# Kernel tuning notes

Measured on AMD Instinct MI355X. Metric: run time of the kernel, lower is better.

The kernel has to match this reference:

```python
import jax, jax.numpy as jnp
import numpy as np

EPS = 1e-5

def setup_inputs() -> dict:
    key = jax.random.key(0)
    ks = jax.random.split(key, 8)
    B, C, H, W = 8, 128, 128, 128
    return {
        "x1": jax.random.normal(ks[0], (B, C, H, W), jnp.float32),
        "x2": jax.random.normal(ks[1], (B, C, H, W), jnp.float32),
        "se_w1": jax.random.normal(ks[2], (C // 4, 2 * C), jnp.float32) * 0.05,
        "se_w2": jax.random.normal(ks[3], (2 * C, C // 4), jnp.float32) * 0.05,
        "conv_w": jax.random.normal(ks[4], (C, 2 * C, 3, 3), jnp.float32) * 0.05,
        "bn_gamma": jnp.ones((C,), jnp.float32),
        "bn_beta": jnp.zeros((C,), jnp.float32),
        "bn_mean": jax.random.normal(ks[5], (C,), jnp.float32) * 0.1,
        "bn_var": jax.random.uniform(ks[6], (C,), jnp.float32, 0.5, 1.5),
        "gamma": jax.random.uniform(ks[7], (1,), jnp.float32),
    }

def reference(x1, x2, se_w1, se_w2, conv_w, bn_gamma, bn_beta, bn_mean, bn_var, gamma):
    B, C, H, W = x1.shape
    x = jnp.concatenate([x1, x2], axis=1)                      # [B,2C,H,W]
    # SE gate: global avg pool -> Linear/ReLU/Linear/Sigmoid
    avg = jnp.mean(x, axis=(2, 3))                             # [B,2C]
    h = jax.nn.relu(avg @ se_w1.T)                             # [B,C//4]
    se = jax.nn.sigmoid(h @ se_w2.T)                           # [B,2C]
    x = x * se[:, :, None, None]
    # ConvBNReLU (3x3, pad 1, eval-mode BN)
    x = jax.lax.conv_general_dilated(
        x, conv_w, window_strides=(1, 1), padding="SAME",
        dimension_numbers=("NCHW", "OIHW", "NCHW"))           # [B,C,H,W]
    inv = bn_gamma / jnp.sqrt(bn_var + EPS)
    x = jax.nn.relu(x * inv[None, :, None, None]
                    + (bn_beta - bn_mean * inv)[None, :, None, None])
    # Channel self-attention with max-subtraction trick
    q = x.reshape(B, C, H * W)                                 # query = key = value
    sim = jnp.einsum("bcn,bdn->bcd", q, q)                     # [B,C,C]
    sim = jnp.max(sim, axis=-1, keepdims=True) - sim
    sim = jax.nn.softmax(sim, axis=-1)
    feat = jnp.einsum("bcd,bdn->bcn", sim, q).reshape(B, C, H, W)
    return gamma * feat + x
```

## Files before the change

kernel.cpp:

```cpp
#include <hip/hip_runtime.h>
#include <math.h>

#define B_   8
#define C_   128
#define C2_  256
#define H_   128
#define W_   128
#define HW_  16384
#define CR_  32
#define EPS_ 1e-5f
#define NS_  32

typedef _Float16 f16;
typedef f16 f16x8 __attribute__((ext_vector_type(8)));
typedef f16 f16x4 __attribute__((ext_vector_type(4)));
typedef float f32x4 __attribute__((ext_vector_type(4)));

__global__ __launch_bounds__(256) void prep_kernel(
    const float* __restrict__ x1, const float* __restrict__ x2,
    float* __restrict__ avg_sums, f16* __restrict__ xs)
{
    __shared__ f16 T[W_ * 136];
    __shared__ float part[C2_];
    int h = blockIdx.x, b = blockIdx.y;
    int tid = threadIdx.x;
    part[tid] = 0.f;
    f16* out = xs + ((size_t)b * H_ + h) * W_ * C2_;
    for (int p = 0; p < 2; ++p) {
        const float* src = p ? x2 : x1;
        __syncthreads();
        for (int idx = tid; idx < C_ * 32; idx += 256) {
            int c = idx >> 5, w4 = (idx & 31) << 2;
            const float4 v = *(const float4*)&src[(((size_t)b * C_ + c) * H_ + h) * W_ + w4];
            float s = v.x + v.y + v.z + v.w;
            s += __shfl_xor(s, 1, 64);  s += __shfl_xor(s, 2, 64);
            s += __shfl_xor(s, 4, 64);  s += __shfl_xor(s, 8, 64);
            s += __shfl_xor(s, 16, 64);
            if ((tid & 31) == 0) part[p * C_ + c] = s;
            int cs = c ^ (8 * ((idx & 31) & 15));
            T[(w4 + 0) * 136 + cs] = (f16)v.x;
            T[(w4 + 1) * 136 + cs] = (f16)v.y;
            T[(w4 + 2) * 136 + cs] = (f16)v.z;
            T[(w4 + 3) * 136 + cs] = (f16)v.w;
        }
        __syncthreads();
        for (int u = tid; u < W_ * 16; u += 256) {
            int w = u >> 4, o = u & 15;
            f16x8 v = *(const f16x8*)&T[w * 136 + ((o * 8) ^ (8 * ((w >> 2) & 15)))];
            *(f16x8*)&out[w * C2_ + p * C_ + o * 8] = v;
        }
    }
    __syncthreads();
    atomicAdd(&avg_sums[b * C2_ + tid], part[tid]);
}

__global__ __launch_bounds__(256) void se_mlp_kernel(
    const float* __restrict__ avg_sums, const float* __restrict__ w1,
    const float* __restrict__ w2, float* __restrict__ se)
{
    __shared__ float s_avg[B_ * C2_];
    __shared__ float s_h[B_ * CR_];
    for (int i = threadIdx.x; i < B_ * C2_; i += 256)
        s_avg[i] = avg_sums[i] * (1.f / (float)HW_);
    __syncthreads();
    {
        int i = threadIdx.x;
        int b = i / CR_, j = i % CR_;
        float s = 0.f;
        for (int k = 0; k < C2_; ++k) s += s_avg[b * C2_ + k] * w1[j * C2_ + k];
        s_h[i] = fmaxf(s, 0.f);
    }
    __syncthreads();
    for (int i = threadIdx.x; i < B_ * C2_; i += 256) {
        int b = i / C2_, c = i % C2_;
        float s = 0.f;
        #pragma unroll
        for (int j = 0; j < CR_; ++j) s += s_h[b * CR_ + j] * w2[c * CR_ + j];
        se[i] = 1.f / (1.f + expf(-s));
    }
}

__global__ __launch_bounds__(256) void wt_build_kernel(
    const float* __restrict__ conv_w, f16* __restrict__ wt)
{
    int idx = blockIdx.x * 256 + threadIdx.x;
    int ci = idx & 31;
    int co = (idx >> 5) & 127;
    int cc = (idx >> 12) & 7;
    int t  = idx >> 15;
    wt[idx] = (f16)conv_w[((size_t)co * C2_ + cc * 32 + ci) * 9 + t];
}

__global__ __launch_bounds__(256, 2) void conv_mfma_kernel(
    const f16* __restrict__ xs, const f16* __restrict__ wt,
    const float* __restrict__ se,
    const float* __restrict__ bn_gamma, const float* __restrict__ bn_beta,
    const float* __restrict__ bn_mean, const float* __restrict__ bn_var,
    f16* __restrict__ yh, f16* __restrict__ yt)
{
    __shared__ f16 Xs[17408];
    __shared__ __align__(16) f16 seh[C2_];
    int h0 = blockIdx.x * 2, b = blockIdx.y;
    int tid = threadIdx.x;
    int wave = tid >> 6, lane = tid & 63;
    int wn = wave;
    int lr = lane & 15, kg = lane >> 4;
    const f16* xsb = xs + (size_t)b * ((size_t)H_ * W_ * C2_);

    seh[tid] = (f16)se[b * C2_ + tid];

    f32x4 acc[2][8][2];
    #pragma unroll
    for (int o = 0; o < 2; ++o)
        #pragma unroll
        for (int i = 0; i < 8; ++i)
            #pragma unroll
            for (int j = 0; j < 2; ++j)
                #pragma unroll
                for (int r = 0; r < 4; ++r) acc[o][i][j][r] = 0.f;

    f16x8 afb[2][8];
    auto ldaf = [&](int cc, int t, f16x8* dst) {
        const f16* wb = wt + ((size_t)(t * 8 + cc) * C_) * 32;
        #pragma unroll
        for (int i = 0; i < 8; ++i)
            dst[i] = *(const f16x8*)&wb[(i * 16 + lr) * 32 + kg * 8];
    };

    for (int cc = 0; cc < 8; ++cc) {
        __syncthreads();
        ldaf(cc, 0, afb[0]);
        for (int u = tid; u < 4 * 130 * 4; u += 256) {
            int r = u / 520;
            int rem = u - r * 520;
            int col = rem >> 2, q = rem & 3;
            int gh = h0 - 1 + r, gw = col - 1;
            f16x8 v;
            #pragma unroll
            for (int z = 0; z < 8; ++z) v[z] = (f16)0.f;
            if ((unsigned)gh < (unsigned)H_ && (unsigned)gw < (unsigned)W_) {
                v = *(const f16x8*)&xsb[((size_t)(gh * W_ + gw)) * C2_ + cc * 32 + q * 8];
                f16x8 sv = *(const f16x8*)&seh[cc * 32 + q * 8];
                v = v * sv;
            }
            *(f16x8*)&Xs[((r * 4 + q) * 132 + col) * 8] = v;
        }
        __syncthreads();
        #pragma unroll
        for (int t = 0; t < 9; ++t) {
            const int dh = t / 3, dw = t % 3;
            if (t < 8) ldaf(cc, t + 1, afb[(t + 1) & 1]);
            const f16x8* af = afb[t & 1];
            #pragma unroll
            for (int o = 0; o < 2; ++o) {
                int r = o + dh;
                f16x8 bf[2];
                #pragma unroll
                for (int j = 0; j < 2; ++j)
                    bf[j] = *(const f16x8*)&Xs[((r * 4 + kg) * 132 +
                                (wn * 32 + j * 16 + lr + dw)) * 8];
                #pragma unroll
                for (int i = 0; i < 8; ++i)
                    #pragma unroll
                    for (int j = 0; j < 2; ++j)
                        acc[o][i][j] = __builtin_amdgcn_mfma_f32_16x16x32_f16(
                            af[i], bf[j], acc[o][i][j], 0, 0, 0);
            }
        }
    }
    #pragma unroll
    for (int o = 0; o < 2; ++o) {
        __syncthreads();
        #pragma unroll
        for (int i = 0; i < 8; ++i) {
            int cb = i * 16 + kg * 4;
            float inv[4], add[4];
            #pragma unroll
            for (int r = 0; r < 4; ++r) {
                int c = cb + r;
                inv[r] = bn_gamma[c] * rsqrtf(bn_var[c] + EPS_);
                add[r] = bn_beta[c] - bn_mean[c] * inv[r];
            }
            #pragma unroll
            for (int j = 0; j < 2; ++j) {
                int n = wn * 32 + j * 16 + lr;
                f16x4 tv;
                #pragma unroll
                for (int r = 0; r < 4; ++r) {
                    float v = fmaxf(acc[o][i][j][r] * inv[r] + add[r], 0.f);
                    tv[r] = (f16)v;
                    yh[((size_t)b * C_ + cb + r) * HW_ + (h0 + o) * W_ + n] = (f16)v;
                }
                *(f16x4*)&Xs[n * 136 + cb] = tv;
            }
        }
        __syncthreads();
        for (int u = tid; u < 128 * 16; u += 256) {
            int n = u >> 4, o8 = u & 15;
            f16x8 v = *(const f16x8*)&Xs[n * 136 + o8 * 8];
            *(f16x8*)&yt[((size_t)b * HW_ + (h0 + o) * W_ + n) * C_ + o8 * 8] = v;
        }
    }
}

__global__ __launch_bounds__(512) void sim_mfma_kernel(
    const f16* __restrict__ yh, float* __restrict__ simp)
{
    int ns = blockIdx.x, b = blockIdx.y;
    int tid = threadIdx.x, wave = tid >> 6, lane = tid & 63;
    int wm = wave >> 2, wn = wave & 3;
    int lr = lane & 15, kg = lane >> 4;
    const f16* Y = yh + (size_t)b * C_ * HW_;
    int n0 = ns * (HW_ / NS_);

    f32x4 acc[4][2];
    #pragma unroll
    for (int i = 0; i < 4; ++i)
        #pragma unroll
        for (int j = 0; j < 2; ++j)
            #pragma unroll
            for (int r = 0; r < 4; ++r) acc[i][j][r] = 0.f;

    for (int kk = 0; kk < 16; ++kk) {
        int k = n0 + kk * 32 + kg * 8;
        f16x8 af[4], bf[2];
        #pragma unroll
        for (int i = 0; i < 4; ++i)
            af[i] = *(const f16x8*)&Y[(size_t)(wm * 64 + i * 16 + lr) * HW_ + k];
        #pragma unroll
        for (int j = 0; j < 2; ++j)
            bf[j] = *(const f16x8*)&Y[(size_t)(wn * 32 + j * 16 + lr) * HW_ + k];
        #pragma unroll
        for (int i = 0; i < 4; ++i)
            #pragma unroll
            for (int j = 0; j < 2; ++j)
                acc[i][j] = __builtin_amdgcn_mfma_f32_16x16x32_f16(af[i], bf[j], acc[i][j], 0, 0, 0);
    }
    float* dst = simp + (size_t)(ns * B_ + b) * C_ * C_;
    #pragma unroll
    for (int i = 0; i < 4; ++i)
        #pragma unroll
        for (int j = 0; j < 2; ++j)
            #pragma unroll
            for (int r = 0; r < 4; ++r)
                dst[(wm * 64 + i * 16 + kg * 4 + r) * C_ + wn * 32 + j * 16 + lr] = acc[i][j][r];
}

__global__ __launch_bounds__(128) void softmax_kernel(
    const float* __restrict__ simp, f16* __restrict__ Ph)
{
    int bc = blockIdx.x;
    int b = bc / C_;
    int d = threadIdx.x;
    float s = 0.f;
    for (int ns = 0; ns < NS_; ++ns)
        s += simp[((size_t)(ns * B_ + b) * C_ + (bc % C_)) * C_ + d];
    float v = -s;
    float m = v;
    #pragma unroll
    for (int off = 32; off > 0; off >>= 1) m = fmaxf(m, __shfl_xor(m, off, 64));
    __shared__ float sm[2], ss[2];
    int wid = threadIdx.x >> 6;
    if ((threadIdx.x & 63) == 0) sm[wid] = m;
    __syncthreads();
    m = fmaxf(sm[0], sm[1]);
    float p = expf(v - m);
    float sum = p;
    #pragma unroll
    for (int off = 32; off > 0; off >>= 1) sum += __shfl_xor(sum, off, 64);
    if ((threadIdx.x & 63) == 0) ss[wid] = sum;
    __syncthreads();
    sum = ss[0] + ss[1];
    Ph[(size_t)bc * C_ + d] = (f16)(p / sum);
}

__global__ __launch_bounds__(256) void feat_mfma_kernel(
    const f16* __restrict__ Ph, const f16* __restrict__ yt,
    const f16* __restrict__ yh,
    const float* __restrict__ gamma, float* __restrict__ out)
{
    int nt = blockIdx.x, b = blockIdx.y;
    int tid = threadIdx.x, wave = tid >> 6, lane = tid & 63;
    int wm = wave >> 1, wn = wave & 1;
    int lr = lane & 15, kg = lane >> 4;
    int n0 = nt * 128;
    const f16* Pb = Ph + (size_t)b * C_ * C_;
    const f16* Yt = yt + (size_t)b * HW_ * C_;

    f32x4 acc[4][4];
    #pragma unroll
    for (int i = 0; i < 4; ++i)
        #pragma unroll
        for (int j = 0; j < 4; ++j)
            #pragma unroll
            for (int r = 0; r < 4; ++r) acc[i][j][r] = 0.f;

    #pragma unroll
    for (int kk = 0; kk < 4; ++kk) {
        int k = kk * 32 + kg * 8;
        f16x8 af[4], bf[4];
        #pragma unroll
        for (int i = 0; i < 4; ++i)
            af[i] = *(const f16x8*)&Pb[(wm * 64 + i * 16 + lr) * C_ + k];
        #pragma unroll
        for (int j = 0; j < 4; ++j)
            bf[j] = *(const f16x8*)&Yt[(size_t)(n0 + wn * 64 + j * 16 + lr) * C_ + k];
        #pragma unroll
        for (int i = 0; i < 4; ++i)
            #pragma unroll
            for (int j = 0; j < 4; ++j)
                acc[i][j] = __builtin_amdgcn_mfma_f32_16x16x32_f16(af[i], bf[j], acc[i][j], 0, 0, 0);
    }
    float g = gamma[0];
    #pragma unroll
    for (int i = 0; i < 4; ++i) {
        int cb = wm * 64 + i * 16 + kg * 4;
        #pragma unroll
        for (int j = 0; j < 4; ++j) {
            int n = n0 + wn * 64 + j * 16 + lr;
            #pragma unroll
            for (int r = 0; r < 4; ++r) {
                float res = (float)yh[((size_t)b * C_ + cb + r) * HW_ + n];
                out[((size_t)b * C_ + cb + r) * HW_ + n] = g * acc[i][j][r] + res;
            }
        }
    }
}

extern "C" void kernel_launch(void* const* d_in, const int* in_sizes, int n_in,
                              void* d_out, int out_size, void* d_ws, size_t ws_size,
                              hipStream_t stream)
{
    const float* x1       = (const float*)d_in[0];
    const float* x2       = (const float*)d_in[1];
    const float* se_w1    = (const float*)d_in[2];
    const float* se_w2    = (const float*)d_in[3];
    const float* conv_w   = (const float*)d_in[4];
    const float* bn_gamma = (const float*)d_in[5];
    const float* bn_beta  = (const float*)d_in[6];
    const float* bn_mean  = (const float*)d_in[7];
    const float* bn_var   = (const float*)d_in[8];
    const float* gamma    = (const float*)d_in[9];
    float* out = (float*)d_out;

    char* ws = (char*)d_ws;
    float* avg  = (float*)(ws);
    float* se   = (float*)(ws + 8192);
    f16*   Ph   = (f16*)  (ws + 16384);
    f16*   wt   = (f16*)  (ws + 278528);
    f16*   xs   = (f16*)  (ws + 1048576);
    float* simp = (float*)(ws + 1048576);
    f16*   yh   = (f16*)  (ws + 68157440);
    f16*   yt   = (f16*)  (ws + 101711872);

    hipMemsetAsync(avg, 0, B_ * C2_ * sizeof(float), stream);
    prep_kernel<<<dim3(H_, B_), 256, 0, stream>>>(x1, x2, avg, xs);
    se_mlp_kernel<<<dim3(1), 256, 0, stream>>>(avg, se_w1, se_w2, se);
    wt_build_kernel<<<dim3(1152), 256, 0, stream>>>(conv_w, wt);
    conv_mfma_kernel<<<dim3(H_ / 2, B_), 256, 0, stream>>>(
        xs, wt, se, bn_gamma, bn_beta, bn_mean, bn_var, yh, yt);
    sim_mfma_kernel<<<dim3(NS_, B_), 512, 0, stream>>>(yh, simp);
    softmax_kernel<<<dim3(B_ * C_), 128, 0, stream>>>(simp, Ph);
    feat_mfma_kernel<<<dim3(HW_ / 128, B_), 256, 0, stream>>>(Ph, yt, yh, gamma, out);
}
```

Measured before the change: 389.0 us.

## Stage conv weights in LDS and compute four output rows per block

Adds a new 512-thread conv kernel that copies all 9 taps of each 32-channel weight chunk into padded shared memory. Each block computes 4 output rows, and each wave owns one row and half the width, so weight reads are reused across rows instead of reloaded from global memory per wave. It reorders the packed weight layout to cc-major to match. The yt output is now written directly as f16x4 stores instead of going through an LDS transpose, and the old kernel stays as a fallback if the large dynamic LDS request is refused. The roughly 142KB LDS request limits occupancy to one block per CU, and the non-coalesced yt stores could cost bandwidth.

```diff
diff --git a/kernel.cpp b/kernel.cpp
--- a/kernel.cpp
+++ b/kernel.cpp
@@ -86,9 +86,115 @@
     int idx = blockIdx.x * 256 + threadIdx.x;
     int ci = idx & 31;
     int co = (idx >> 5) & 127;
-    int cc = (idx >> 12) & 7;
-    int t  = idx >> 15;
+    int tt = idx >> 12;
+    int cc = tt / 9, t = tt - cc * 9;
     wt[idx] = (f16)conv_w[((size_t)co * C2_ + cc * 32 + ci) * 9 + t];
+}
+
+#define WS_F16  46080
+#define XS_F16  24960
+#define SMEM_BYTES 142592
+
+__global__ __launch_bounds__(512, 2) void conv_mfma_big(
+    const f16* __restrict__ xs, const f16* __restrict__ wt,
+    const float* __restrict__ se,
+    const float* __restrict__ bn_gamma, const float* __restrict__ bn_beta,
+    const float* __restrict__ bn_mean, const float* __restrict__ bn_var,
+    f16* __restrict__ yh, f16* __restrict__ yt)
+{
+    extern __shared__ __align__(16) f16 smem[];
+    f16* Ws  = smem;
+    f16* Xs  = smem + WS_F16;
+    f16* seh = smem + WS_F16 + XS_F16;
+
+    int h0 = blockIdx.x * 4, b = blockIdx.y;
+    int tid = threadIdx.x;
+    int wave = tid >> 6, lane = tid & 63;
+    int orow = wave >> 1, nh = wave & 1;
+    int lr = lane & 15, kg = lane >> 4;
+    const f16* xsb = xs + (size_t)b * ((size_t)H_ * W_ * C2_);
+    const f16* wtb = wt;
+
+    if (tid < 256) seh[tid] = (f16)se[b * C2_ + tid];
+
+    f32x4 acc[8][4];
+    #pragma unroll
+    for (int i = 0; i < 8; ++i)
+        #pragma unroll
+        for (int j = 0; j < 4; ++j)
+            #pragma unroll
+            for (int r = 0; r < 4; ++r) acc[i][j][r] = 0.f;
+
+    for (int cc = 0; cc < 8; ++cc) {
+        __syncthreads();
+        {
+            const f16* wsrc = wtb + (size_t)cc * (9 * 128 * 32);
+            for (int u = tid; u < 4608; u += 512) {
+                int kgu = u & 3, co = (u >> 2) & 127, t = u >> 9;
+                f16x8 w = *(const f16x8*)&wsrc[(t * 128 + co) * 32 + kgu * 8];
+                *(f16x8*)&Ws[(t * 128 + co) * 40 + kgu * 8] = w;
+            }
+        }
+        for (int u = tid; u < 3120; u += 512) {
+            int r = u / 520;
+            int rem = u - r * 520;
+            int col = rem >> 2, q = rem & 3;
+            int gh = h0 - 1 + r, gw = col - 1;
+            f16x8 v;
+            #pragma unroll
+            for (int z = 0; z < 8; ++z) v[z] = (f16)0.f;
+            if ((unsigned)gh < (unsigned)H_ && (unsigned)gw < (unsigned)W_) {
+                v = *(const f16x8*)&xsb[((size_t)(gh * W_ + gw)) * C2_ + cc * 32 + q * 8];
+                f16x8 sv = *(const f16x8*)&seh[cc * 32 + q * 8];
+                v = v * sv;
+            }
+            *(f16x8*)&Xs[((r * 4 + q) * 130 + col) * 8] = v;
+        }
+        __syncthreads();
+        #pragma unroll
+        for (int t = 0; t < 9; ++t) {
+            const int dh = t / 3, dw = t % 3;
+            const int rr = orow + dh;
+            f16x8 af[8], bf[4];
+            #pragma unroll
+            for (int i = 0; i < 8; ++i)
+                af[i] = *(const f16x8*)&Ws[(t * 128 + i * 16 + lr) * 40 + kg * 8];
+            #pragma unroll
+            for (int j = 0; j < 4; ++j)
+                bf[j] = *(const f16x8*)&Xs[((rr * 4 + kg) * 130 +
+                            (nh * 64 + j * 16 + lr + dw)) * 8];
+            #pragma unroll
+            for (int i = 0; i < 8; ++i)
+                #pragma unroll
+                for (int j = 0; j < 4; ++j)
+                    acc[i][j] = __builtin_amdgcn_mfma_f32_16x16x32_f16(
+                        af[i], bf[j], acc[i][j], 0, 0, 0);
+        }
+    }
+    int h = h0 + orow;
+    #pragma unroll
+    for (int i = 0; i < 8; ++i) {
+        int cb = i * 16 + kg * 4;
+        float inv[4], add[4];
+        #pragma unroll
+        for (int r = 0; r < 4; ++r) {
+            int c = cb + r;
+            inv[r] = bn_gamma[c] * rsqrtf(bn_var[c] + EPS_);
+            add[r] = bn_beta[c] - bn_mean[c] * inv[r];
+        }
+        #pragma unroll
+        for (int j = 0; j < 4; ++j) {
+            int n = nh * 64 + j * 16 + lr;
+            f16x4 tv;
+            #pragma unroll
+            for (int r = 0; r < 4; ++r) {
+                float v = fmaxf(acc[i][j][r] * inv[r] + add[r], 0.f);
+                tv[r] = (f16)v;
+                yh[((size_t)b * C_ + cb + r) * HW_ + h * W_ + n] = (f16)v;
+            }
+            *(f16x4*)&yt[((size_t)b * HW_ + h * W_ + n) * C_ + cb] = tv;
+        }
+    }
 }
 
 __global__ __launch_bounds__(256, 2) void conv_mfma_kernel(
@@ -121,7 +227,7 @@
 
     f16x8 afb[2][8];
     auto ldaf = [&](int cc, int t, f16x8* dst) {
-        const f16* wb = wt + ((size_t)(t * 8 + cc) * C_) * 32;
+        const f16* wb = wt + ((size_t)(cc * 9 + t) * C_) * 32;
         #pragma unroll
         for (int i = 0; i < 8; ++i)
             dst[i] = *(const f16x8*)&wb[(i * 16 + lr) * 32 + kg * 8];
@@ -170,7 +276,6 @@
     }
     #pragma unroll
     for (int o = 0; o < 2; ++o) {
-        __syncthreads();
         #pragma unroll
         for (int i = 0; i < 8; ++i) {
             int cb = i * 16 + kg * 4;
@@ -191,14 +296,8 @@
                     tv[r] = (f16)v;
                     yh[((size_t)b * C_ + cb + r) * HW_ + (h0 + o) * W_ + n] = (f16)v;
                 }
-                *(f16x4*)&Xs[n * 136 + cb] = tv;
-            }
-        }
-        __syncthreads();
-        for (int u = tid; u < 128 * 16; u += 256) {
-            int n = u >> 4, o8 = u & 15;
-            f16x8 v = *(const f16x8*)&Xs[n * 136 + o8 * 8];
-            *(f16x8*)&yt[((size_t)b * HW_ + (h0 + o) * W_ + n) * C_ + o8 * 8] = v;
+                *(f16x4*)&yt[((size_t)b * HW_ + (h0 + o) * W_ + n) * C_ + cb] = tv;
+            }
         }
     }
 }
@@ -357,8 +456,18 @@
     prep_kernel<<<dim3(H_, B_), 256, 0, stream>>>(x1, x2, avg, xs);
     se_mlp_kernel<<<dim3(1), 256, 0, stream>>>(avg, se_w1, se_w2, se);
     wt_build_kernel<<<dim3(1152), 256, 0, stream>>>(conv_w, wt);
-    conv_mfma_kernel<<<dim3(H_ / 2, B_), 256, 0, stream>>>(
-        xs, wt, se, bn_gamma, bn_beta, bn_mean, bn_var, yh, yt);
+
+    hipError_t aerr = hipFuncSetAttribute(
+        (const void*)conv_mfma_big,
+        hipFuncAttributeMaxDynamicSharedMemorySize, SMEM_BYTES);
+    if (aerr == hipSuccess) {
+        conv_mfma_big<<<dim3(H_ / 4, B_), 512, SMEM_BYTES, stream>>>(
+            xs, wt, se, bn_gamma, bn_beta, bn_mean, bn_var, yh, yt);
+    } else {
+        conv_mfma_kernel<<<dim3(H_ / 2, B_), 256, 0, stream>>>(
+            xs, wt, se, bn_gamma, bn_beta, bn_mean, bn_var, yh, yt);
+    }
+
     sim_mfma_kernel<<<dim3(NS_, B_), 512, 0, stream>>>(yh, simp);
     softmax_kernel<<<dim3(B_ * C_), 128, 0, stream>>>(simp, Ph);
     feat_mfma_kernel<<<dim3(HW_ / 128, B_), 256, 0, stream>>>(Ph, yt, yh, gamma, out);
```

Result: no change. 394.4 us (+1.4%).

## Stage conv weights in LDS with 4-row tiles and register prefetch; fuse weight repack

Applied to the files above, without the earlier changes.

The conv kernel now handles four output rows per block with 512 threads. It stages each 32-channel chunk of weights and the SE-scaled input halo in dynamic LDS, and prefetches the next chunk into registers while the MFMAs run. Weights that were reloaded from global memory per tap are now reused from LDS across more output rows. The weight repack moves into the prep kernel, and the memset and atomics are replaced by per-row partial sums that a per-batch SE MLP reduces. The cost is about 139 KB of LDS per block, so only one block fits per CU, along with high register pressure from the prefetch buffers.

```diff
diff --git a/kernel.cpp b/kernel.cpp
--- a/kernel.cpp
+++ b/kernel.cpp
@@ -18,13 +18,13 @@
 
 __global__ __launch_bounds__(256) void prep_kernel(
     const float* __restrict__ x1, const float* __restrict__ x2,
-    float* __restrict__ avg_sums, f16* __restrict__ xs)
+    const float* __restrict__ conv_w,
+    float* __restrict__ avgp, f16* __restrict__ xs, f16* __restrict__ wt)
 {
     __shared__ f16 T[W_ * 136];
     __shared__ float part[C2_];
     int h = blockIdx.x, b = blockIdx.y;
     int tid = threadIdx.x;
-    part[tid] = 0.f;
     f16* out = xs + ((size_t)b * H_ + h) * W_ * C2_;
     for (int p = 0; p < 2; ++p) {
         const float* src = p ? x2 : x1;
@@ -51,154 +51,192 @@
         }
     }
     __syncthreads();
-    atomicAdd(&avg_sums[b * C2_ + tid], part[tid]);
+    avgp[((size_t)h * B_ + b) * C2_ + tid] = part[tid];
+    {
+        int base = (b * H_ + h) * 288;
+        for (int i = tid; i < 288; i += 256) {
+            int idx = base + i;
+            int ci = idx & 31;
+            int co = (idx >> 5) & 127;
+            int tt = idx >> 12;
+            int cc = tt / 9, t = tt - cc * 9;
+            wt[idx] = (f16)conv_w[((size_t)co * C2_ + cc * 32 + ci) * 9 + t];
+        }
+    }
 }
 
 __global__ __launch_bounds__(256) void se_mlp_kernel(
-    const float* __restrict__ avg_sums, const float* __restrict__ w1,
+    const float* __restrict__ avgp, const float* __restrict__ w1,
     const float* __restrict__ w2, float* __restrict__ se)
 {
-    __shared__ float s_avg[B_ * C2_];
-    __shared__ float s_h[B_ * CR_];
-    for (int i = threadIdx.x; i < B_ * C2_; i += 256)
-        s_avg[i] = avg_sums[i] * (1.f / (float)HW_);
+    int b = blockIdx.x;
+    __shared__ float s_avg[C2_];
+    __shared__ float s_h[CR_];
+    float s = 0.f;
+    for (int h = 0; h < H_; ++h)
+        s += avgp[((size_t)h * B_ + b) * C2_ + threadIdx.x];
+    s_avg[threadIdx.x] = s * (1.f / (float)HW_);
     __syncthreads();
     {
-        int i = threadIdx.x;
-        int b = i / CR_, j = i % CR_;
-        float s = 0.f;
-        for (int k = 0; k < C2_; ++k) s += s_avg[b * C2_ + k] * w1[j * C2_ + k];
-        s_h[i] = fmaxf(s, 0.f);
-    }
-    __syncthreads();
-    for (int i = threadIdx.x; i < B_ * C2_; i += 256) {
-        int b = i / C2_, c = i % C2_;
-        float s = 0.f;
-        #pragma unroll
-        for (int j = 0; j < CR_; ++j) s += s_h[b * CR_ + j] * w2[c * CR_ + j];
-        se[i] = 1.f / (1.f + expf(-s));
-    }
-}
-
-__global__ __launch_bounds__(256) void wt_build_kernel(
-    const float* __restrict__ conv_w, f16* __restrict__ wt)
-{
-    int idx = blockIdx.x * 256 + threadIdx.x;
-    int ci = idx & 31;
-    int co = (idx >> 5) & 127;
-    int cc = (idx >> 12) & 7;
-    int t  = idx >> 15;
-    wt[idx] = (f16)conv_w[((size_t)co * C2_ + cc * 32 + ci) * 9 + t];
-}
-
-__global__ __launch_bounds__(256, 2) void conv_mfma_kernel(
+        int j = threadIdx.x >> 3, sub = threadIdx.x & 7;
+        float a = 0.f;
+        #pragma unroll 8
+        for (int k = sub * 32; k < sub * 32 + 32; ++k) a += s_avg[k] * w1[j * C2_ + k];
+        a += __shfl_xor(a, 1, 64); a += __shfl_xor(a, 2, 64); a += __shfl_xor(a, 4, 64);
+        if (sub == 0) s_h[j] = fmaxf(a, 0.f);
+    }
+    __syncthreads();
+    float o = 0.f;
+    #pragma unroll
+    for (int j = 0; j < CR_; ++j) o += s_h[j] * w2[threadIdx.x * CR_ + j];
+    se[b * C2_ + threadIdx.x] = 1.f / (1.f + expf(-o));
+}
+
+#define WS_F16  46080
+#define XS_F16  24960
+#define SMEM_BYTES 142592
+
+__global__ __launch_bounds__(512, 2) void conv_mfma_big(
     const f16* __restrict__ xs, const f16* __restrict__ wt,
     const float* __restrict__ se,
     const float* __restrict__ bn_gamma, const float* __restrict__ bn_beta,
     const float* __restrict__ bn_mean, const float* __restrict__ bn_var,
     f16* __restrict__ yh, f16* __restrict__ yt)
 {
-    __shared__ f16 Xs[17408];
-    __shared__ __align__(16) f16 seh[C2_];
-    int h0 = blockIdx.x * 2, b = blockIdx.y;
+    extern __shared__ __align__(16) f16 smem[];
+    f16* Ws  = smem;
+    f16* Xs  = smem + WS_F16;
+    f16* seh = smem + WS_F16 + XS_F16;
+
+    int h0 = blockIdx.x * 4, b = blockIdx.y;
     int tid = threadIdx.x;
     int wave = tid >> 6, lane = tid & 63;
-    int wn = wave;
+    int orow = wave >> 1, nh = wave & 1;
     int lr = lane & 15, kg = lane >> 4;
     const f16* xsb = xs + (size_t)b * ((size_t)H_ * W_ * C2_);
 
-    seh[tid] = (f16)se[b * C2_ + tid];
-
-    f32x4 acc[2][8][2];
-    #pragma unroll
-    for (int o = 0; o < 2; ++o)
-        #pragma unroll
-        for (int i = 0; i < 8; ++i)
-            #pragma unroll
-            for (int j = 0; j < 2; ++j)
-                #pragma unroll
-                for (int r = 0; r < 4; ++r) acc[o][i][j][r] = 0.f;
-
-    f16x8 afb[2][8];
-    auto ldaf = [&](int cc, int t, f16x8* dst) {
-        const f16* wb = wt + ((size_t)(t * 8 + cc) * C_) * 32;
-        #pragma unroll
-        for (int i = 0; i < 8; ++i)
-            dst[i] = *(const f16x8*)&wb[(i * 16 + lr) * 32 + kg * 8];
+    if (tid < 256) seh[tid] = (f16)se[b * C2_ + tid];
+    __syncthreads();
+
+    f32x4 acc[8][4];
+    #pragma unroll
+    for (int i = 0; i < 8; ++i)
+        #pragma unroll
+        for (int j = 0; j < 4; ++j)
+            #pragma unroll
+            for (int r = 0; r < 4; ++r) acc[i][j][r] = 0.f;
+
+    f16x8 wreg[9], xreg[7];
+
+    auto preload = [&](int cc) {
+        const f16* wsrc = wt + (size_t)cc * 36864;
+        #pragma unroll
+        for (int k = 0; k < 9; ++k)
+            wreg[k] = *(const f16x8*)&wsrc[(k * 512 + tid) * 8];
+        #pragma unroll
+        for (int k = 0; k < 7; ++k) {
+            int u = k * 512 + tid;
+            f16x8 v;
+            #pragma unroll
+            for (int z = 0; z < 8; ++z) v[z] = (f16)0.f;
+            if (u < 3120) {
+                int r = u / 520, rem = u - r * 520;
+                int col = rem >> 2, q = rem & 3;
+                int gh = h0 - 1 + r, gw = col - 1;
+                if ((unsigned)gh < (unsigned)H_ && (unsigned)gw < (unsigned)W_) {
+                    v = *(const f16x8*)&xsb[((size_t)(gh * W_ + gw)) * C2_ + cc * 32 + q * 8];
+                    f16x8 sv = *(const f16x8*)&seh[cc * 32 + q * 8];
+                    v = v * sv;
+                }
+            }
+            xreg[k] = v;
+        }
     };
 
+    preload(0);
+
     for (int cc = 0; cc < 8; ++cc) {
         __syncthreads();
-        ldaf(cc, 0, afb[0]);
-        for (int u = tid; u < 4 * 130 * 4; u += 256) {
-            int r = u / 520;
-            int rem = u - r * 520;
-            int col = rem >> 2, q = rem & 3;
-            int gh = h0 - 1 + r, gw = col - 1;
-            f16x8 v;
-            #pragma unroll
-            for (int z = 0; z < 8; ++z) v[z] = (f16)0.f;
-            if ((unsigned)gh < (unsigned)H_ && (unsigned)gw < (unsigned)W_) {
-                v = *(const f16x8*)&xsb[((size_t)(gh * W_ + gw)) * C2_ + cc * 32 + q * 8];
-                f16x8 sv = *(const f16x8*)&seh[cc * 32 + q * 8];
-                v = v * sv;
+        #pragma unroll
+        for (int k = 0; k < 9; ++k) {
+            int u = k * 512 + tid;
+            *(f16x8*)&Ws[(u >> 2) * 40 + (u & 3) * 8] = wreg[k];
+        }
+        #pragma unroll
+        for (int k = 0; k < 7; ++k) {
+            int u = k * 512 + tid;
+            if (u < 3120) {
+                int r = u / 520, rem = u - r * 520;
+                int col = rem >> 2, q = rem & 3;
+                *(f16x8*)&Xs[((r * 4 + q) * 130 + col) * 8] = xreg[k];
             }
-            *(f16x8*)&Xs[((r * 4 + q) * 132 + col) * 8] = v;
-        }
-        __syncthreads();
+        }
+        __syncthreads();
+        if (cc < 7) preload(cc + 1);
         #pragma unroll
         for (int t = 0; t < 9; ++t) {
             const int dh = t / 3, dw = t % 3;
-            if (t < 8) ldaf(cc, t + 1, afb[(t + 1) & 1]);
-            const f16x8* af = afb[t & 1];
-            #pragma unroll
-            for (int o = 0; o < 2; ++o) {
-                int r = o + dh;
-                f16x8 bf[2];
+            const int rr = orow + dh;
+            f16x8 bf[4];
+            #pragma unroll
+            for (int j = 0; j < 4; ++j)
+                bf[j] = *(const f16x8*)&Xs[((rr * 4 + kg) * 130 +
+                            (nh * 64 + j * 16 + lr + dw)) * 8];
+            #pragma unroll
+            for (int half = 0; half < 2; ++half) {
+                f16x8 af[4];
                 #pragma unroll
-                for (int j = 0; j < 2; ++j)
-                    bf[j] = *(const f16x8*)&Xs[((r * 4 + kg) * 132 +
-                                (wn * 32 + j * 16 + lr + dw)) * 8];
+                for (int i2 = 0; i2 < 4; ++i2)
+                    af[i2] = *(const f16x8*)&Ws[(t * 128 + (half * 4 + i2) * 16 + lr) * 40 + kg * 8];
                 #pragma unroll
-                for (int i = 0; i < 8; ++i)
+                for (int i2 = 0; i2 < 4; ++i2)
                     #pragma unroll
-                    for (int j = 0; j < 2; ++j)
-                        acc[o][i][j] = __builtin_amdgcn_mfma_f32_16x16x32_f16(
-                            af[i], bf[j], acc[o][i][j], 0, 0, 0);
+                    for (int j = 0; j < 4; ++j)
+                        acc[half * 4 + i2][j] = __builtin_amdgcn_mfma_f32_16x16x32_f16(
+                            af[i2], bf[j], acc[half * 4 + i2][j], 0, 0, 0);
             }
         }
     }
-    #pragma unroll
-    for (int o = 0; o < 2; ++o) {
-        __syncthreads();
-        #pragma unroll
-        for (int i = 0; i < 8; ++i) {
-            int cb = i * 16 + kg * 4;
-            float inv[4], add[4];
+    int h = h0 + orow;
+    f16x4 tvv[8][4];
+    #pragma unroll
+    for (int i = 0; i < 8; ++i) {
+        int cb = i * 16 + kg * 4;
+        float inv[4], add[4];
+        #pragma unroll
+        for (int r = 0; r < 4; ++r) {
+            int c = cb + r;
+            inv[r] = bn_gamma[c] * rsqrtf(bn_var[c] + EPS_);
+            add[r] = bn_beta[c] - bn_mean[c] * inv[r];
+        }
+        #pragma unroll
+        for (int j = 0; j < 4; ++j) {
+            int n = nh * 64 + j * 16 + lr;
+            f16x4 tv;
             #pragma unroll
             for (int r = 0; r < 4; ++r) {
-                int c = cb + r;
-                inv[r] = bn_gamma[c] * rsqrtf(bn_var[c] + EPS_);
-                add[r] = bn_beta[c] - bn_mean[c] * inv[r];
+                float v = fmaxf(acc[i][j][r] * inv[r] + add[r], 0.f);
+                tv[r] = (f16)v;
+                yh[((size_t)b * C_ + cb + r) * HW_ + h * W_ + n] = (f16)v;
             }
-            #pragma unroll
-            for (int j = 0; j < 2; ++j) {
-                int n = wn * 32 + j * 16 + lr;
-                f16x4 tv;
+            tvv[i][j] = tv;
+        }
+    }
+    f16* T = Xs;
+    for (int ro = 0; ro < 4; ++ro) {
+        __syncthreads();
+        if (orow == ro) {
+            #pragma unroll
+            for (int i = 0; i < 8; ++i)
                 #pragma unroll
-                for (int r = 0; r < 4; ++r) {
-                    float v = fmaxf(acc[o][i][j][r] * inv[r] + add[r], 0.f);
-                    tv[r] = (f16)v;
-                    yh[((size_t)b * C_ + cb + r) * HW_ + (h0 + o) * W_ + n] = (f16)v;
-                }
-                *(f16x4*)&Xs[n * 136 + cb] = tv;
-            }
-        }
-        __syncthreads();
-        for (int u = tid; u < 128 * 16; u += 256) {
+                for (int j = 0; j < 4; ++j)
+                    *(f16x4*)&T[(nh * 64 + j * 16 + lr) * 136 + i * 16 + kg * 4] = tvv[i][j];
+        }
+        __syncthreads();
+        for (int u = tid; u < 2048; u += 512) {
             int n = u >> 4, o8 = u & 15;
-            f16x8 v = *(const f16x8*)&Xs[n * 136 + o8 * 8];
-            *(f16x8*)&yt[((size_t)b * HW_ + (h0 + o) * W_ + n) * C_ + o8 * 8] = v;
+            *(f16x8*)&yt[((size_t)b * HW_ + (h0 + ro) * W_ + n) * C_ + o8 * 8] =
+                *(const f16x8*)&T[n * 136 + o8 * 8];
         }
     }
 }
@@ -344,21 +382,23 @@
     float* out = (float*)d_out;
 
     char* ws = (char*)d_ws;
-    float* avg  = (float*)(ws);
     float* se   = (float*)(ws + 8192);
     f16*   Ph   = (f16*)  (ws + 16384);
     f16*   wt   = (f16*)  (ws + 278528);
     f16*   xs   = (f16*)  (ws + 1048576);
     float* simp = (float*)(ws + 1048576);
     f16*   yh   = (f16*)  (ws + 68157440);
+    float* avgp = (float*)(ws + 68157440);
     f16*   yt   = (f16*)  (ws + 101711872);
 
-    hipMemsetAsync(avg, 0, B_ * C2_ * sizeof(float), stream);
-    prep_kernel<<<dim3(H_, B_), 256, 0, stream>>>(x1, x2, avg, xs);
-    se_mlp_kernel<<<dim3(1), 256, 0, stream>>>(avg, se_w1, se_w2, se);
-    wt_build_kernel<<<dim3(1152), 256, 0, stream>>>(conv_w, wt);
-    conv_mfma_kernel<<<dim3(H_ / 2, B_), 256, 0, stream>>>(
+    prep_kernel<<<dim3(H_, B_), 256, 0, stream>>>(x1, x2, conv_w, avgp, xs, wt);
+    se_mlp_kernel<<<dim3(B_), 256, 0, stream>>>(avgp, se_w1, se_w2, se);
+
+    hipFuncSetAttribute((const void*)conv_mfma_big,
+        hipFuncAttributeMaxDynamicSharedMemorySize, SMEM_BYTES);
+    conv_mfma_big<<<dim3(H_ / 4, B_), 512, SMEM_BYTES, stream>>>(
         xs, wt, se, bn_gamma, bn_beta, bn_mean, bn_var, yh, yt);
+
     sim_mfma_kernel<<<dim3(NS_, B_), 512, 0, stream>>>(yh, simp);
     softmax_kernel<<<dim3(B_ * C_), 128, 0, stream>>>(simp, Ph);
     feat_mfma_kernel<<<dim3(HW_ / 128, B_), 256, 0, stream>>>(Ph, yt, yh, gamma, out);
```

New measurement: 373.8 us. -3.9%, faster.
